# Performance work log

Measured on AMD Instinct MI355X. Metric: run time of the kernel, lower is better.

## Reference

```python
import jax, jax.numpy as jnp
import numpy as np

DIM = 384
HD = 64
SCALE = float(HD ** 0.5)


def _linear_params(key, out_f, in_f):
    kw, kb = jax.random.split(key)
    bound = 1.0 / np.sqrt(in_f)
    W = jax.random.uniform(kw, (out_f, in_f), jnp.float32, -bound, bound)
    b = jax.random.uniform(kb, (out_f,), jnp.float32, -bound, bound)
    return W, b


def setup_inputs() -> dict:
    key = jax.random.key(0)
    ks = jax.random.split(key, 12)
    N = 8192
    situation = jax.random.normal(ks[0], (DIM,), jnp.float32)
    turn_embeddings = jax.random.normal(ks[1], (N, DIM), jnp.float32)
    bilinear_scores = jax.random.normal(ks[2], (N,), jnp.float32)
    Wt, bt = _linear_params(ks[3], HD, DIM + 1)      # turn_proj
    Ws, bs = _linear_params(ks[4], HD, DIM)          # situation_proj
    Wsaq, bsaq = _linear_params(ks[5], HD, HD)
    Wsak, bsak = _linear_params(ks[6], HD, HD)
    Wsav, bsav = _linear_params(ks[7], HD, HD)
    Wcq, bcq = _linear_params(ks[8], HD, HD)
    Wck, bck = _linear_params(ks[9], HD, HD)
    Wcv, bcv = _linear_params(ks[10], HD, HD)
    # score_head is zero-initialized in the module; use small random values so
    # the output is non-trivial for kernel correctness testing.
    Wsc, bsc = _linear_params(ks[11], 1, HD)
    residual_gate = jnp.float32(-5.0)
    return dict(situation=situation, turn_embeddings=turn_embeddings,
                bilinear_scores=bilinear_scores,
                Wt=Wt, bt=bt, Ws=Ws, bs=bs,
                Wsaq=Wsaq, bsaq=bsaq, Wsak=Wsak, bsak=bsak, Wsav=Wsav, bsav=bsav,
                Wcq=Wcq, bcq=bcq, Wck=Wck, bck=bck, Wcv=Wcv, bcv=bcv,
                Wsc=Wsc, bsc=bsc, residual_gate=residual_gate)


def reference(situation, turn_embeddings, bilinear_scores,
              Wt, bt, Ws, bs,
              Wsaq, bsaq, Wsak, bsak, Wsav, bsav,
              Wcq, bcq, Wck, bck, Wcv, bcv,
              Wsc, bsc, residual_gate):
    # [N, dim+1] = [turn_embedding; bilinear_score]
    turn_features = jnp.concatenate([turn_embeddings, bilinear_scores[:, None]], axis=-1)
    turn_hidden = turn_features @ Wt.T + bt                      # [N, HD]
    # self-attention among turns (dropout = identity, eval mode)
    sa_q = turn_hidden @ Wsaq.T + bsaq
    sa_k = turn_hidden @ Wsak.T + bsak
    sa_v = turn_hidden @ Wsav.T + bsav
    sa_weights = jax.nn.softmax((sa_q @ sa_k.T) / SCALE, axis=-1)  # [N, N]
    turn_hidden = turn_hidden + sa_weights @ sa_v
    # sigmoid cross-attention against the single situation vector
    sit_hidden = (situation @ Ws.T + bs)[None, :]                # [1, HD]
    ca_q = turn_hidden @ Wcq.T + bcq                             # [N, HD]
    ca_k = sit_hidden @ Wck.T + bck                              # [1, HD]
    ca_v = sit_hidden @ Wcv.T + bcv                              # [1, HD]
    ca_weights = jax.nn.sigmoid((ca_q @ ca_k.T) / SCALE)         # [N, 1]
    combined = turn_hidden + ca_weights * ca_v                   # [N, HD]
    attention_scores = (combined @ Wsc.T + bsc)[:, 0]            # [N]
    gate = jax.nn.sigmoid(residual_gate)
    return (1.0 - gate) * bilinear_scores + gate * attention_scores
```

## Files before the change

### kernel.cpp

```cpp
#include <hip/hip_runtime.h>
#include <hip/hip_bf16.h>

typedef __attribute__((ext_vector_type(8))) short short8;
typedef __attribute__((ext_vector_type(4))) float f32x4;

__device__ __forceinline__ short f2bf(float x) {
  union { float f; unsigned u; } a; a.f = x;
  unsigned r = (a.u + 0x7FFFu + ((a.u >> 16) & 1u)) >> 16;
  return (short)r;
}
__device__ __forceinline__ float bf2f(short x) {
  union { unsigned u; float f; } a; a.u = ((unsigned)(unsigned short)x) << 16;
  return a.f;
}
__device__ __forceinline__ unsigned cvtpk(float lo, float hi) {
  unsigned r;
  asm("v_cvt_pk_bf16_f32 %0, %1, %2" : "=v"(r) : "v"(lo), "v"(hi));
  return r;
}
__device__ __forceinline__ void gload16(const void* g, void* l) {
  __builtin_amdgcn_global_load_lds((const __attribute__((address_space(1))) unsigned int*)g,
                                   (__attribute__((address_space(3))) unsigned int*)l, 16, 0, 0);
}

__global__ __launch_bounds__(256) void ca_setup2(
    const float* __restrict__ Wt, short* __restrict__ Wtb, float* __restrict__ wcol,
    const float* __restrict__ sit, const float* __restrict__ Ws, const float* __restrict__ bs,
    const float* __restrict__ Wck, const float* __restrict__ bck, const float* __restrict__ Wcv,
    const float* __restrict__ bcv, const float* __restrict__ Wcq, const float* __restrict__ bcq,
    const float* __restrict__ Wsc, float* __restrict__ u_ws, float* __restrict__ scal) {
  const int bid = blockIdx.x, t = threadIdx.x;
  if (bid < 97) {
    int idx = bid * 256 + t;
    if (idx < 24576) {
      int r = idx / 384, c = idx % 384;
      Wtb[idx] = f2bf(Wt[r * 385 + c]);
    } else if (idx < 24640) {
      wcol[idx - 24576] = Wt[(idx - 24576) * 385 + 384];
    }
    return;
  }
  __shared__ float part[4][64];
  __shared__ float sh[64], ck[64], cv[64];
  int j = t & 63, p = t >> 6;
  float a = 0.f;
  for (int d = p * 96; d < p * 96 + 96; ++d) a += Ws[j * 384 + d] * sit[d];
  part[p][j] = a;
  __syncthreads();
  if (t < 64) sh[t] = part[0][t] + part[1][t] + part[2][t] + part[3][t] + bs[t];
  __syncthreads();
  if (t < 64) {
    float kk = bck[t], vv = bcv[t];
    for (int d = 0; d < 64; ++d) { kk += Wck[t * 64 + d] * sh[d]; vv += Wcv[t * 64 + d] * sh[d]; }
    ck[t] = kk; cv[t] = vv;
  }
  __syncthreads();
  if (t < 64) {
    float uu = 0.f;
    for (int jj = 0; jj < 64; ++jj) uu += Wcq[jj * 64 + t] * ck[jj];
    u_ws[t] = uu;
  }
  if (t == 0) {
    float c0 = 0.f, cw = 0.f;
    for (int jj = 0; jj < 64; ++jj) { c0 += bcq[jj] * ck[jj]; cw += cv[jj] * Wsc[jj]; }
    scal[0] = c0; scal[1] = cw;
  }
}

__global__ __launch_bounds__(256) void ca_proj2(
    const float* __restrict__ te, const float* __restrict__ bil,
    const short* __restrict__ Wtb, const float* __restrict__ wcol2, const float* __restrict__ bt,
    const float* __restrict__ Wsaq, const float* __restrict__ bq,
    const float* __restrict__ Wsak, const float* __restrict__ bk2,
    const float* __restrict__ Wsav, const float* __restrict__ bv,
    short* __restrict__ hb, short* __restrict__ qb, short* __restrict__ kb,
    short* __restrict__ vt, int N) {
  __shared__ float Pp[8192];
  __shared__ short Hl[32][72];
  __shared__ short Vt[64][40];
  const int t = threadIdx.x, lane = t & 63, w = t >> 6;
  const int g = lane >> 4, li = lane & 15;
  const int i0 = blockIdx.x * 32;

  f32x4 acc[2][4];
#pragma unroll
  for (int qs = 0; qs < 2; ++qs)
#pragma unroll
    for (int n = 0; n < 4; ++n) acc[qs][n] = (f32x4){0.f, 0.f, 0.f, 0.f};
  const int kw = w * 96;
#pragma unroll
  for (int ks = 0; ks < 3; ++ks) {
    short8 af[2];
#pragma unroll
    for (int qs = 0; qs < 2; ++qs) {
      const float* ap = te + (size_t)(i0 + qs * 16 + li) * 384 + kw + ks * 32 + g * 8;
      float4 a0 = *(const float4*)ap;
      float4 a1 = *(const float4*)(ap + 4);
      af[qs][0] = f2bf(a0.x); af[qs][1] = f2bf(a0.y); af[qs][2] = f2bf(a0.z); af[qs][3] = f2bf(a0.w);
      af[qs][4] = f2bf(a1.x); af[qs][5] = f2bf(a1.y); af[qs][6] = f2bf(a1.z); af[qs][7] = f2bf(a1.w);
    }
#pragma unroll
    for (int n = 0; n < 4; ++n) {
      short8 bf = *(const short8*)&Wtb[(size_t)(n * 16 + li) * 384 + kw + ks * 32 + g * 8];
      acc[0][n] = __builtin_amdgcn_mfma_f32_16x16x32_bf16(af[0], bf, acc[0][n], 0, 0, 0);
      acc[1][n] = __builtin_amdgcn_mfma_f32_16x16x32_bf16(af[1], bf, acc[1][n], 0, 0, 0);
    }
  }
#pragma unroll
  for (int qs = 0; qs < 2; ++qs)
#pragma unroll
    for (int n = 0; n < 4; ++n)
      *(f32x4*)&Pp[((w * 8 + qs * 4 + n) * 64 + lane) * 4] = acc[qs][n];
  __syncthreads();
#pragma unroll
  for (int ss = 0; ss < 2; ++ss) {
    int s = t + ss * 256;
    int qs2 = s >> 8, n2 = (s >> 6) & 3, lane2 = s & 63;
    int g2 = lane2 >> 4, li2 = lane2 & 15;
    int base = (qs2 * 4 + n2) * 256 + lane2 * 4;
    f32x4 v0 = *(const f32x4*)&Pp[base];
    f32x4 v1 = *(const f32x4*)&Pp[base + 2048];
    f32x4 v2 = *(const f32x4*)&Pp[base + 4096];
    f32x4 v3 = *(const f32x4*)&Pp[base + 6144];
    int col = n2 * 16 + li2;
    float wc = wcol2[col], bb = bt[col];
#pragma unroll
    for (int r = 0; r < 4; ++r) {
      int row = qs2 * 16 + g2 * 4 + r;
      float val = v0[r] + v1[r] + v2[r] + v3[r] + bb + bil[i0 + row] * wc;
      Hl[row][col] = f2bf(val);
    }
  }
  __syncthreads();
  {
    int row = t >> 3, seg = t & 7;
    *(uint4*)&hb[(size_t)(i0 + row) * 64 + seg * 8] = *(uint4*)&Hl[row][seg * 8];
  }
  short8 ha[2][2];
#pragma unroll
  for (int qs = 0; qs < 2; ++qs)
#pragma unroll
    for (int ks = 0; ks < 2; ++ks)
      ha[qs][ks] = *(const short8*)&Hl[qs * 16 + li][ks * 32 + g * 8];
  const float* Wm[3] = {Wsaq, Wsak, Wsav};
  f32x4 pacc[3][2];
#pragma unroll
  for (int m = 0; m < 3; ++m)
#pragma unroll
    for (int qs = 0; qs < 2; ++qs) pacc[m][qs] = (f32x4){0.f, 0.f, 0.f, 0.f};
#pragma unroll
  for (int m = 0; m < 3; ++m)
#pragma unroll
    for (int ks = 0; ks < 2; ++ks) {
      const float* wp = Wm[m] + (size_t)(w * 16 + li) * 64 + ks * 32 + g * 8;
      float4 b0 = *(const float4*)wp;
      float4 b1 = *(const float4*)(wp + 4);
      short8 bf;
      bf[0] = f2bf(b0.x); bf[1] = f2bf(b0.y); bf[2] = f2bf(b0.z); bf[3] = f2bf(b0.w);
      bf[4] = f2bf(b1.x); bf[5] = f2bf(b1.y); bf[6] = f2bf(b1.z); bf[7] = f2bf(b1.w);
      pacc[m][0] = __builtin_amdgcn_mfma_f32_16x16x32_bf16(ha[0][ks], bf, pacc[m][0], 0, 0, 0);
      pacc[m][1] = __builtin_amdgcn_mfma_f32_16x16x32_bf16(ha[1][ks], bf, pacc[m][1], 0, 0, 0);
    }
  const int col = w * 16 + li;
  const float QSC = 0.18033688011112042f;
  {
    float bbq = bq[col], bbk = bk2[col], bbv = bv[col];
#pragma unroll
    for (int qs = 0; qs < 2; ++qs)
#pragma unroll
      for (int r = 0; r < 4; ++r) {
        int row = i0 + qs * 16 + g * 4 + r;
        qb[(size_t)row * 64 + col] = f2bf((pacc[0][qs][r] + bbq) * QSC);
        kb[(size_t)row * 64 + col] = f2bf(pacc[1][qs][r] + bbk);
        Vt[col][qs * 16 + g * 4 + r] = f2bf(pacc[2][qs][r] + bbv);
      }
  }
  __syncthreads();
  {
    int c = t >> 2, seg = t & 3;
    *(uint4*)&vt[(size_t)c * N + i0 + seg * 8] = *(uint4*)&Vt[c][seg * 8];
  }
}

__global__ __launch_bounds__(256, 2) void ca_attn4(
    const short* __restrict__ qb, const short* __restrict__ kb, const short* __restrict__ vt,
    short* __restrict__ pO, float* __restrict__ pL, int N) {
  __shared__ short Kl[2][4096];
  __shared__ short Vl[2][4096];
  __shared__ short Pl[4][32][72];
  const int t = threadIdx.x, lane = t & 63, wid = t >> 6;
  const int g = lane >> 4, li = lane & 15;
  const int bid = blockIdx.x;
  const int sp = (bid >> 1) & 7;
  const int qblk = (bid >> 4) * 2 + (bid & 1);
  const int i0 = qblk * 128 + wid * 32;
  const int k0 = sp * (N >> 3);
  const int ntil = N >> 9;

  const short* ksrc = kb + ((size_t)(wid * 16 + li)) * 64 + g * 8;
  const short* vsrc0 = vt + (size_t)(li + ((2 * wid) & 3) * 16) * N + (wid >> 1) * 32 + g * 8;
  const short* vsrc1 = vt + (size_t)(li + ((2 * wid + 1) & 3) * 16) * N + (wid >> 1) * 32 + g * 8;

#define STAGE_TILE(b, j0)                                                \
  do {                                                                   \
    gload16(ksrc + (size_t)(j0) * 64,       &Kl[b][(2 * wid) * 512]);    \
    gload16(ksrc + (size_t)(j0) * 64 + 32,  &Kl[b][(2 * wid + 1) * 512]);\
    gload16(vsrc0 + (j0),                   &Vl[b][(2 * wid) * 512]);    \
    gload16(vsrc1 + (j0),                   &Vl[b][(2 * wid + 1) * 512]);\
  } while (0)

  short8 qa[2][2];
#pragma unroll
  for (int qs = 0; qs < 2; ++qs)
#pragma unroll
    for (int ks = 0; ks < 2; ++ks)
      qa[qs][ks] = *(const short8*)&qb[(size_t)(i0 + qs * 16 + li) * 64 + g * 8 + ks * 32];

  f32x4 acc[2][4];
  float rs[2] = {0.f, 0.f};
#pragma unroll
  for (int qs = 0; qs < 2; ++qs)
#pragma unroll
    for (int n = 0; n < 4; ++n) acc[qs][n] = (f32x4){0.f, 0.f, 0.f, 0.f};

  STAGE_TILE(0, k0);
  asm volatile("s_waitcnt vmcnt(0)" ::: "memory");

  for (int tt = 0; tt < ntil; ++tt) {
    const int cur = tt & 1;
    __builtin_amdgcn_s_barrier();
    if (tt + 1 < ntil) STAGE_TILE(cur ^ 1, k0 + (tt + 1) * 64);

    f32x4 s4[2][4];
#pragma unroll
    for (int qs = 0; qs < 2; ++qs)
#pragma unroll
      for (int t4 = 0; t4 < 4; ++t4) s4[qs][t4] = (f32x4){0.f, 0.f, 0.f, 0.f};
    __builtin_amdgcn_s_setprio(1);
#pragma unroll
    for (int ks = 0; ks < 2; ++ks)
#pragma unroll
      for (int t4 = 0; t4 < 4; ++t4) {
        short8 kf = *(const short8*)&Kl[cur][(t4 * 2 + ks) * 512 + lane * 8];
        s4[0][t4] = __builtin_amdgcn_mfma_f32_16x16x32_bf16(kf, qa[0][ks], s4[0][t4], 0, 0, 0);
        s4[1][t4] = __builtin_amdgcn_mfma_f32_16x16x32_bf16(kf, qa[1][ks], s4[1][t4], 0, 0, 0);
      }
    __builtin_amdgcn_s_setprio(0);
#pragma unroll
    for (int qs = 0; qs < 2; ++qs) {
#pragma unroll
      for (int t4 = 0; t4 < 4; ++t4) {
        float p0, p1, p2, p3;
        asm("v_exp_f32 %0, %1" : "=v"(p0) : "v"(s4[qs][t4][0]));
        asm("v_exp_f32 %0, %1" : "=v"(p1) : "v"(s4[qs][t4][1]));
        asm("v_exp_f32 %0, %1" : "=v"(p2) : "v"(s4[qs][t4][2]));
        asm("v_exp_f32 %0, %1" : "=v"(p3) : "v"(s4[qs][t4][3]));
        rs[qs] += (p0 + p1) + (p2 + p3);
        uint2 wv;
        wv.x = cvtpk(p0, p1);
        wv.y = cvtpk(p2, p3);
        *(uint2*)&Pl[wid][qs * 16 + li][t4 * 16 + g * 4] = wv;
      }
    }
    asm volatile("s_waitcnt lgkmcnt(0)" ::: "memory");
    short8 pa[2][2];
#pragma unroll
    for (int qs = 0; qs < 2; ++qs)
#pragma unroll
      for (int ks2 = 0; ks2 < 2; ++ks2)
        pa[qs][ks2] = *(const short8*)&Pl[wid][qs * 16 + li][g * 8 + ks2 * 32];
    __builtin_amdgcn_s_setprio(1);
#pragma unroll
    for (int ks2 = 0; ks2 < 2; ++ks2)
#pragma unroll
      for (int dt = 0; dt < 4; ++dt) {
        short8 vf = *(const short8*)&Vl[cur][(ks2 * 4 + dt) * 512 + lane * 8];
        acc[0][dt] = __builtin_amdgcn_mfma_f32_16x16x32_bf16(pa[0][ks2], vf, acc[0][dt], 0, 0, 0);
        acc[1][dt] = __builtin_amdgcn_mfma_f32_16x16x32_bf16(pa[1][ks2], vf, acc[1][dt], 0, 0, 0);
      }
    __builtin_amdgcn_s_setprio(0);
    asm volatile("s_waitcnt vmcnt(0)" ::: "memory");
  }

  const size_t base = (size_t)sp * N + i0;
#pragma unroll
  for (int qs = 0; qs < 2; ++qs) {
#pragma unroll
    for (int dt = 0; dt < 4; ++dt)
#pragma unroll
      for (int r = 0; r < 4; ++r)
        pO[(base + qs * 16 + g * 4 + r) * 64 + li + dt * 16] = f2bf(acc[qs][dt][r]);
    float r2 = rs[qs] + __shfl_xor(rs[qs], 16, 64);
    r2 += __shfl_xor(r2, 32, 64);
    if (lane < 16) pL[(size_t)sp * N + i0 + qs * 16 + lane] = r2;
  }
#undef STAGE_TILE
}

__global__ __launch_bounds__(256) void ca_merge(
    const short* __restrict__ hb, const short* __restrict__ pO, const float* __restrict__ pL,
    const float* __restrict__ u_ws, const float* __restrict__ scal,
    const float* __restrict__ bil, const float* __restrict__ Wsc,
    const float* __restrict__ bsc_p, const float* __restrict__ rgate_p,
    float* __restrict__ out, int N) {
  const int t = threadIdx.x;
  const int row = blockIdx.x * 32 + (t >> 3), e = t & 7, d0 = e * 8;
  float L = 0.f;
#pragma unroll
  for (int sp = 0; sp < 8; ++sp) L += pL[(size_t)sp * N + row];
  float o[8];
#pragma unroll
  for (int i = 0; i < 8; ++i) o[i] = 0.f;
#pragma unroll
  for (int sp = 0; sp < 8; ++sp) {
    short8 ov = *(const short8*)&pO[((size_t)sp * N + row) * 64 + d0];
#pragma unroll
    for (int i = 0; i < 8; ++i) o[i] += bf2f(ov[i]);
  }
  const float invL = 1.f / L;
  short8 hv = *(const short8*)&hb[(size_t)row * 64 + d0];
  float s1 = 0.f, s2 = 0.f;
#pragma unroll
  for (int i = 0; i < 8; ++i) {
    float h2 = bf2f(hv[i]) + o[i] * invL;
    s1 += h2 * u_ws[d0 + i];
    s2 += h2 * Wsc[d0 + i];
  }
#pragma unroll
  for (int mask = 1; mask < 8; mask <<= 1) {
    s1 += __shfl_xor(s1, mask, 64);
    s2 += __shfl_xor(s2, mask, 64);
  }
  if (e == 0) {
    float gate = 1.f / (1.f + __expf(-rgate_p[0]));
    float caw = 1.f / (1.f + __expf(-(s1 + scal[0]) * 0.125f));
    float score = s2 + caw * scal[1] + bsc_p[0];
    out[row] = (1.f - gate) * bil[row] + gate * score;
  }
}

extern "C" void kernel_launch(void* const* d_in, const int* in_sizes, int n_in,
                              void* d_out, int out_size, void* d_ws, size_t ws_size,
                              hipStream_t stream) {
  const float* sit  = (const float*)d_in[0];
  const float* te   = (const float*)d_in[1];
  const float* bil  = (const float*)d_in[2];
  const float* Wt   = (const float*)d_in[3];
  const float* bt   = (const float*)d_in[4];
  const float* Ws   = (const float*)d_in[5];
  const float* bs   = (const float*)d_in[6];
  const float* Wsaq = (const float*)d_in[7];
  const float* bsaq = (const float*)d_in[8];
  const float* Wsak = (const float*)d_in[9];
  const float* bsak = (const float*)d_in[10];
  const float* Wsav = (const float*)d_in[11];
  const float* bsav = (const float*)d_in[12];
  const float* Wcq  = (const float*)d_in[13];
  const float* bcq  = (const float*)d_in[14];
  const float* Wck  = (const float*)d_in[15];
  const float* bck  = (const float*)d_in[16];
  const float* Wcv  = (const float*)d_in[17];
  const float* bcv  = (const float*)d_in[18];
  const float* Wsc  = (const float*)d_in[19];
  const float* bsc  = (const float*)d_in[20];
  const float* rgate= (const float*)d_in[21];
  const int N = in_sizes[2];

  char* w = (char*)d_ws;
  size_t off = 0;
  short* hbuf  = (short*)(w + off); off += (size_t)N * 64 * 2;
  short* qbuf  = (short*)(w + off); off += (size_t)N * 64 * 2;
  short* kbuf  = (short*)(w + off); off += (size_t)N * 64 * 2;
  short* vtbuf = (short*)(w + off); off += (size_t)N * 64 * 2;
  float* u_ws  = (float*)(w + off); off += 64 * 4;
  float* scal  = (float*)(w + off); off += 4 * 4;
  short* Wtb   = (short*)(w + off); off += 24576 * 2;
  float* wcol  = (float*)(w + off); off += 64 * 4;
  short* pO    = (short*)(w + off); off += (size_t)8 * N * 64 * 2;
  float* pL    = (float*)(w + off); off += (size_t)8 * N * 4;

  ca_setup2<<<98, 256, 0, stream>>>(Wt, Wtb, wcol, sit, Ws, bs, Wck, bck, Wcv, bcv,
                                    Wcq, bcq, Wsc, u_ws, scal);
  ca_proj2<<<N / 32, 256, 0, stream>>>(te, bil, Wtb, wcol, bt, Wsaq, bsaq, Wsak, bsak,
                                       Wsav, bsav, hbuf, qbuf, kbuf, vtbuf, N);
  ca_attn4<<<N / 16, 256, 0, stream>>>(qbuf, kbuf, vtbuf, pO, pL, N);
  ca_merge<<<N / 32, 256, 0, stream>>>(hbuf, pO, pL, u_ws, scal, bil, Wsc, bsc, rgate,
                                       (float*)d_out, N);
}
```

Measured before the change: 56.44 us.

## Fuse setup into projection and merge into attention via last-block counter

Removes the separate setup kernel by folding the situation-vector precomputation into an extra block of the projection kernel, which now converts Wt to bf16 on the fly instead of reading a pre-converted copy. The merge kernel is eliminated: each attention block atomically increments a per-query-block counter, and the last of the eight key-split blocks reduces the partial outputs and writes the final scores. Partial outputs are stored in an MFMA-fragment layout with packed bf16 conversion to make writes contiguous. This cuts two kernel launches and their gaps, at the cost of redundant Wt conversion per block, uncoalesced strided Wt reads, and a serialized tail reduction in the last-arriving blocks.

```diff
diff --git a/kernel.cpp b/kernel.cpp
--- a/kernel.cpp
+++ b/kernel.cpp
@@ -23,62 +23,54 @@
                                    (__attribute__((address_space(3))) unsigned int*)l, 16, 0, 0);
 }
 
-__global__ __launch_bounds__(256) void ca_setup2(
-    const float* __restrict__ Wt, short* __restrict__ Wtb, float* __restrict__ wcol,
-    const float* __restrict__ sit, const float* __restrict__ Ws, const float* __restrict__ bs,
-    const float* __restrict__ Wck, const float* __restrict__ bck, const float* __restrict__ Wcv,
-    const float* __restrict__ bcv, const float* __restrict__ Wcq, const float* __restrict__ bcq,
-    const float* __restrict__ Wsc, float* __restrict__ u_ws, float* __restrict__ scal) {
-  const int bid = blockIdx.x, t = threadIdx.x;
-  if (bid < 97) {
-    int idx = bid * 256 + t;
-    if (idx < 24576) {
-      int r = idx / 384, c = idx % 384;
-      Wtb[idx] = f2bf(Wt[r * 385 + c]);
-    } else if (idx < 24640) {
-      wcol[idx - 24576] = Wt[(idx - 24576) * 385 + 384];
-    }
-    return;
-  }
-  __shared__ float part[4][64];
-  __shared__ float sh[64], ck[64], cv[64];
-  int j = t & 63, p = t >> 6;
-  float a = 0.f;
-  for (int d = p * 96; d < p * 96 + 96; ++d) a += Ws[j * 384 + d] * sit[d];
-  part[p][j] = a;
-  __syncthreads();
-  if (t < 64) sh[t] = part[0][t] + part[1][t] + part[2][t] + part[3][t] + bs[t];
-  __syncthreads();
-  if (t < 64) {
-    float kk = bck[t], vv = bcv[t];
-    for (int d = 0; d < 64; ++d) { kk += Wck[t * 64 + d] * sh[d]; vv += Wcv[t * 64 + d] * sh[d]; }
-    ck[t] = kk; cv[t] = vv;
-  }
-  __syncthreads();
-  if (t < 64) {
-    float uu = 0.f;
-    for (int jj = 0; jj < 64; ++jj) uu += Wcq[jj * 64 + t] * ck[jj];
-    u_ws[t] = uu;
-  }
-  if (t == 0) {
-    float c0 = 0.f, cw = 0.f;
-    for (int jj = 0; jj < 64; ++jj) { c0 += bcq[jj] * ck[jj]; cw += cv[jj] * Wsc[jj]; }
-    scal[0] = c0; scal[1] = cw;
-  }
-}
-
-__global__ __launch_bounds__(256) void ca_proj2(
+__global__ __launch_bounds__(256) void ca_proj3(
     const float* __restrict__ te, const float* __restrict__ bil,
-    const short* __restrict__ Wtb, const float* __restrict__ wcol2, const float* __restrict__ bt,
+    const float* __restrict__ Wt, const float* __restrict__ bt,
     const float* __restrict__ Wsaq, const float* __restrict__ bq,
     const float* __restrict__ Wsak, const float* __restrict__ bk2,
     const float* __restrict__ Wsav, const float* __restrict__ bv,
     short* __restrict__ hb, short* __restrict__ qb, short* __restrict__ kb,
-    short* __restrict__ vt, int N) {
+    short* __restrict__ vt,
+    const float* __restrict__ sit, const float* __restrict__ Ws, const float* __restrict__ bs,
+    const float* __restrict__ Wck, const float* __restrict__ bck,
+    const float* __restrict__ Wcv, const float* __restrict__ bcv,
+    const float* __restrict__ Wcq, const float* __restrict__ bcq,
+    const float* __restrict__ Wsc, float* __restrict__ u_ws, float* __restrict__ scal,
+    unsigned* __restrict__ cnt, int N) {
   __shared__ float Pp[8192];
   __shared__ short Hl[32][72];
   __shared__ short Vt[64][40];
-  const int t = threadIdx.x, lane = t & 63, w = t >> 6;
+  __shared__ float part[4][64];
+  __shared__ float sh[64], ck[64], cv[64];
+  const int t = threadIdx.x;
+  if ((int)blockIdx.x == (N >> 5)) {
+    if (t < 64) cnt[t] = 0;
+    int j = t & 63, p = t >> 6;
+    float a = 0.f;
+    for (int d = p * 96; d < p * 96 + 96; ++d) a += Ws[j * 384 + d] * sit[d];
+    part[p][j] = a;
+    __syncthreads();
+    if (t < 64) sh[t] = part[0][t] + part[1][t] + part[2][t] + part[3][t] + bs[t];
+    __syncthreads();
+    if (t < 64) {
+      float kk = bck[t], vv = bcv[t];
+      for (int d = 0; d < 64; ++d) { kk += Wck[t * 64 + d] * sh[d]; vv += Wcv[t * 64 + d] * sh[d]; }
+      ck[t] = kk; cv[t] = vv;
+    }
+    __syncthreads();
+    if (t < 64) {
+      float uu = 0.f;
+      for (int jj = 0; jj < 64; ++jj) uu += Wcq[jj * 64 + t] * ck[jj];
+      u_ws[t] = uu;
+    }
+    if (t == 0) {
+      float c0 = 0.f, cw = 0.f;
+      for (int jj = 0; jj < 64; ++jj) { c0 += bcq[jj] * ck[jj]; cw += cv[jj] * Wsc[jj]; }
+      scal[0] = c0; scal[1] = cw;
+    }
+    return;
+  }
+  const int lane = t & 63, w = t >> 6;
   const int g = lane >> 4, li = lane & 15;
   const int i0 = blockIdx.x * 32;
 
@@ -101,7 +93,10 @@
     }
 #pragma unroll
     for (int n = 0; n < 4; ++n) {
-      short8 bf = *(const short8*)&Wtb[(size_t)(n * 16 + li) * 384 + kw + ks * 32 + g * 8];
+      short8 bf;
+      const float* wp = Wt + (size_t)(n * 16 + li) * 385 + kw + ks * 32 + g * 8;
+#pragma unroll
+      for (int jj = 0; jj < 8; ++jj) bf[jj] = f2bf(wp[jj]);
       acc[0][n] = __builtin_amdgcn_mfma_f32_16x16x32_bf16(af[0], bf, acc[0][n], 0, 0, 0);
       acc[1][n] = __builtin_amdgcn_mfma_f32_16x16x32_bf16(af[1], bf, acc[1][n], 0, 0, 0);
     }
@@ -123,7 +118,7 @@
     f32x4 v2 = *(const f32x4*)&Pp[base + 4096];
     f32x4 v3 = *(const f32x4*)&Pp[base + 6144];
     int col = n2 * 16 + li2;
-    float wc = wcol2[col], bb = bt[col];
+    float wc = Wt[(size_t)col * 385 + 384], bb = bt[col];
 #pragma unroll
     for (int r = 0; r < 4; ++r) {
       int row = qs2 * 16 + g2 * 4 + r;
@@ -182,12 +177,17 @@
   }
 }
 
-__global__ __launch_bounds__(256, 2) void ca_attn4(
+__global__ __launch_bounds__(256, 2) void ca_attn5(
     const short* __restrict__ qb, const short* __restrict__ kb, const short* __restrict__ vt,
-    short* __restrict__ pO, float* __restrict__ pL, int N) {
+    unsigned* __restrict__ pOu, float* __restrict__ pL,
+    const short* __restrict__ hb, const float* __restrict__ u_ws, const float* __restrict__ scal,
+    const float* __restrict__ bil, const float* __restrict__ Wsc,
+    const float* __restrict__ bsc_p, const float* __restrict__ rgate_p,
+    unsigned* __restrict__ cnt, float* __restrict__ out, int N) {
   __shared__ short Kl[2][4096];
   __shared__ short Vl[2][4096];
   __shared__ short Pl[4][32][72];
+  __shared__ int lastFlag;
   const int t = threadIdx.x, lane = t & 63, wid = t >> 6;
   const int g = lane >> 4, li = lane & 15;
   const int bid = blockIdx.x;
@@ -282,60 +282,85 @@
     asm volatile("s_waitcnt vmcnt(0)" ::: "memory");
   }
 
-  const size_t base = (size_t)sp * N + i0;
+  const size_t ob = ((size_t)sp * (N >> 5) + (i0 >> 5)) * 2;
 #pragma unroll
   for (int qs = 0; qs < 2; ++qs) {
 #pragma unroll
-    for (int dt = 0; dt < 4; ++dt)
-#pragma unroll
-      for (int r = 0; r < 4; ++r)
-        pO[(base + qs * 16 + g * 4 + r) * 64 + li + dt * 16] = f2bf(acc[qs][dt][r]);
+    for (int dt = 0; dt < 4; ++dt) {
+      uint2 wv;
+      wv.x = cvtpk(acc[qs][dt][0], acc[qs][dt][1]);
+      wv.y = cvtpk(acc[qs][dt][2], acc[qs][dt][3]);
+      *(uint2*)&pOu[((ob + qs) * 4 + dt) * 128 + lane * 2] = wv;
+    }
     float r2 = rs[qs] + __shfl_xor(rs[qs], 16, 64);
     r2 += __shfl_xor(r2, 32, 64);
     if (lane < 16) pL[(size_t)sp * N + i0 + qs * 16 + lane] = r2;
   }
 #undef STAGE_TILE
-}
-
-__global__ __launch_bounds__(256) void ca_merge(
-    const short* __restrict__ hb, const short* __restrict__ pO, const float* __restrict__ pL,
-    const float* __restrict__ u_ws, const float* __restrict__ scal,
-    const float* __restrict__ bil, const float* __restrict__ Wsc,
-    const float* __restrict__ bsc_p, const float* __restrict__ rgate_p,
-    float* __restrict__ out, int N) {
-  const int t = threadIdx.x;
-  const int row = blockIdx.x * 32 + (t >> 3), e = t & 7, d0 = e * 8;
-  float L = 0.f;
-#pragma unroll
-  for (int sp = 0; sp < 8; ++sp) L += pL[(size_t)sp * N + row];
-  float o[8];
-#pragma unroll
-  for (int i = 0; i < 8; ++i) o[i] = 0.f;
-#pragma unroll
-  for (int sp = 0; sp < 8; ++sp) {
-    short8 ov = *(const short8*)&pO[((size_t)sp * N + row) * 64 + d0];
-#pragma unroll
-    for (int i = 0; i < 8; ++i) o[i] += bf2f(ov[i]);
-  }
-  const float invL = 1.f / L;
-  short8 hv = *(const short8*)&hb[(size_t)row * 64 + d0];
-  float s1 = 0.f, s2 = 0.f;
-#pragma unroll
-  for (int i = 0; i < 8; ++i) {
-    float h2 = bf2f(hv[i]) + o[i] * invL;
-    s1 += h2 * u_ws[d0 + i];
-    s2 += h2 * Wsc[d0 + i];
-  }
-#pragma unroll
-  for (int mask = 1; mask < 8; mask <<= 1) {
-    s1 += __shfl_xor(s1, mask, 64);
-    s2 += __shfl_xor(s2, mask, 64);
-  }
-  if (e == 0) {
-    float gate = 1.f / (1.f + __expf(-rgate_p[0]));
-    float caw = 1.f / (1.f + __expf(-(s1 + scal[0]) * 0.125f));
-    float score = s2 + caw * scal[1] + bsc_p[0];
-    out[row] = (1.f - gate) * bil[row] + gate * score;
+
+  __threadfence();
+  __syncthreads();
+  if (t == 0) {
+    unsigned old = atomicAdd(&cnt[qblk], 1u);
+    lastFlag = (old == 7u);
+  }
+  __syncthreads();
+  if (!lastFlag) return;
+  __threadfence();
+
+  const int rp = t >> 3, e = t & 7;
+  const int dt2 = e >> 1, li0 = (e & 1) * 8;
+  const float gate = 1.f / (1.f + __expf(-rgate_p[0]));
+  const float bsc = bsc_p[0], sc0 = scal[0], sc1 = scal[1];
+#pragma unroll
+  for (int pass = 0; pass < 2; ++pass) {
+    const int R0 = qblk * 128 + pass * 64 + rp * 2;
+    const int b32 = R0 >> 5, qs2 = (R0 >> 4) & 1, g2 = (R0 >> 2) & 3;
+    const int rpair = (R0 & 3) >> 1;
+    float o0[8], o1[8], L0 = 0.f, L1 = 0.f;
+#pragma unroll
+    for (int j = 0; j < 8; ++j) { o0[j] = 0.f; o1[j] = 0.f; }
+#pragma unroll
+    for (int sp2 = 0; sp2 < 8; ++sp2) {
+      size_t base = ((((size_t)sp2 * (N >> 5) + b32) * 2 + qs2) * 4 + dt2) * 128
+                    + (g2 * 16 + li0) * 2 + rpair;
+#pragma unroll
+      for (int j = 0; j < 8; ++j) {
+        unsigned u = pOu[base + 2 * j];
+        o0[j] += bf2f((short)(u & 0xffff));
+        o1[j] += bf2f((short)(u >> 16));
+      }
+      L0 += pL[(size_t)sp2 * N + R0];
+      L1 += pL[(size_t)sp2 * N + R0 + 1];
+    }
+    const float iL0 = 1.f / L0, iL1 = 1.f / L1;
+    const int c0 = dt2 * 16 + li0;
+    short8 hv0 = *(const short8*)&hb[(size_t)R0 * 64 + c0];
+    short8 hv1 = *(const short8*)&hb[(size_t)(R0 + 1) * 64 + c0];
+    float s1a = 0.f, s2a = 0.f, s1b = 0.f, s2b = 0.f;
+#pragma unroll
+    for (int j = 0; j < 8; ++j) {
+      float uwsj = u_ws[c0 + j], wscj = Wsc[c0 + j];
+      float h0 = bf2f(hv0[j]) + o0[j] * iL0;
+      float h1 = bf2f(hv1[j]) + o1[j] * iL1;
+      s1a += h0 * uwsj; s2a += h0 * wscj;
+      s1b += h1 * uwsj; s2b += h1 * wscj;
+    }
+#pragma unroll
+    for (int mask = 1; mask < 8; mask <<= 1) {
+      s1a += __shfl_xor(s1a, mask, 64);
+      s2a += __shfl_xor(s2a, mask, 64);
+      s1b += __shfl_xor(s1b, mask, 64);
+      s2b += __shfl_xor(s2b, mask, 64);
+    }
+    if (e == 0) {
+      float cawa = 1.f / (1.f + __expf(-(s1a + sc0) * 0.125f));
+      float cawb = 1.f / (1.f + __expf(-(s1b + sc0) * 0.125f));
+      float scoreA = s2a + cawa * sc1 + bsc;
+      float scoreB = s2b + cawb * sc1 + bsc;
+      out[R0] = (1.f - gate) * bil[R0] + gate * scoreA;
+      out[R0 + 1] = (1.f - gate) * bil[R0 + 1] + gate * scoreB;
+    }
   }
 }
 
@@ -374,16 +399,14 @@
   short* vtbuf = (short*)(w + off); off += (size_t)N * 64 * 2;
   float* u_ws  = (float*)(w + off); off += 64 * 4;
   float* scal  = (float*)(w + off); off += 4 * 4;
-  short* Wtb   = (short*)(w + off); off += 24576 * 2;
-  float* wcol  = (float*)(w + off); off += 64 * 4;
-  short* pO    = (short*)(w + off); off += (size_t)8 * N * 64 * 2;
+  unsigned* cnt= (unsigned*)(w + off); off += 64 * 4;
+  unsigned* pOu= (unsigned*)(w + off); off += (size_t)8 * N * 64 * 2;
   float* pL    = (float*)(w + off); off += (size_t)8 * N * 4;
 
-  ca_setup2<<<98, 256, 0, stream>>>(Wt, Wtb, wcol, sit, Ws, bs, Wck, bck, Wcv, bcv,
-                                    Wcq, bcq, Wsc, u_ws, scal);
-  ca_proj2<<<N / 32, 256, 0, stream>>>(te, bil, Wtb, wcol, bt, Wsaq, bsaq, Wsak, bsak,
-                                       Wsav, bsav, hbuf, qbuf, kbuf, vtbuf, N);
-  ca_attn4<<<N / 16, 256, 0, stream>>>(qbuf, kbuf, vtbuf, pO, pL, N);
-  ca_merge<<<N / 32, 256, 0, stream>>>(hbuf, pO, pL, u_ws, scal, bil, Wsc, bsc, rgate,
-                                       (float*)d_out, N);
-}
+  ca_proj3<<<N / 32 + 1, 256, 0, stream>>>(te, bil, Wt, bt, Wsaq, bsaq, Wsak, bsak,
+                                           Wsav, bsav, hbuf, qbuf, kbuf, vtbuf,
+                                           sit, Ws, bs, Wck, bck, Wcv, bcv, Wcq, bcq, Wsc,
+                                           u_ws, scal, cnt, N);
+  ca_attn5<<<N / 16, 256, 0, stream>>>(qbuf, kbuf, vtbuf, pOu, pL, hbuf, u_ws, scal,
+                                       bil, Wsc, bsc, rgate, cnt, (float*)d_out, N);
+}
```

Result: slower. 134.1 us (+137.6%).
